# Kernel tuning notes

Measured on AMD Instinct MI355X. Metric: run time of the kernel, lower is better.

The kernel has to match this reference:

```python
import jax, jax.numpy as jnp
import numpy as np

PH, PW = 7, 7          # pooled_height, pooled_width
SCALE = 0.0625         # spatial_scale
K = 6                  # static max integer cells per bin side (max bin size = 448*SCALE/7 = 4)


def setup_inputs() -> dict:
    key = jax.random.key(0)
    kf, kb, kx, ky, kw, kh = jax.random.split(key, 6)
    B, C, H, W = 4, 256, 64, 64
    R = 1024
    features = jax.random.normal(kf, (B, C, H, W), dtype=jnp.float32)
    # rois rows: (batch_idx, x1, y1, x2, y2) in image coords (image ~1024px, scale 1/16)
    bidx = jax.random.randint(kb, (R,), 0, B).astype(jnp.float32)
    x1 = jax.random.uniform(kx, (R,), minval=0.0, maxval=576.0)
    y1 = jax.random.uniform(ky, (R,), minval=0.0, maxval=576.0)
    bw = jax.random.uniform(kw, (R,), minval=32.0, maxval=448.0)
    bh = jax.random.uniform(kh, (R,), minval=32.0, maxval=448.0)
    rois = jnp.stack([bidx, x1, y1, x1 + bw, y1 + bh], axis=1)
    return {"features": features, "rois": rois}


def _gather(features, b, hidx, widx, H, W):
    # hidx: [R,PH] int32, widx: [R,PW] int32 -> [R,PH,PW,C]; out-of-bounds reads are zero
    vh = (hidx >= 0) & (hidx < H)
    vw = (widx >= 0) & (widx < W)
    mask = (vh[:, :, None] & vw[:, None, :]).astype(features.dtype)  # [R,PH,PW]
    hc = jnp.clip(hidx, 0, H - 1)
    wc = jnp.clip(widx, 0, W - 1)
    d = features[b[:, None, None], :, hc[:, :, None], wc[:, None, :]]  # [R,PH,PW,C]
    return d * mask[..., None]


def _cell_weights(start, end, s):
    # exact integrals of the two 1D bilinear hat weights over [start,end] clipped to cell [s, s+1]
    y0 = jnp.maximum(start, s)
    yl = jnp.maximum(jnp.minimum(end, s + 1.0), y0)  # empty intersection -> zero weights
    a = y0 - s
    la = yl - s
    g0 = la - 0.5 * la * la - a + 0.5 * a * a  # weight of node at s
    g1 = 0.5 * la * la - 0.5 * a * a           # weight of node at s+1
    return g0, g1


def prroi_pool(features, rois):
    B, C, H, W = features.shape
    R = rois.shape[0]
    dt = features.dtype
    b = rois[:, 0].astype(jnp.int32)
    x1 = rois[:, 1] * SCALE
    y1 = rois[:, 2] * SCALE
    x2 = rois[:, 3] * SCALE
    y2 = rois[:, 4] * SCALE
    roi_w = jnp.maximum(x2 - x1, 0.0)
    roi_h = jnp.maximum(y2 - y1, 0.0)
    bin_w = roi_w / PW
    bin_h = roi_h / PH
    # per-bin continuous windows [ws, we)
    ws_w = x1[:, None] + bin_w[:, None] * jnp.arange(PW, dtype=dt)  # [R,PW]
    ws_h = y1[:, None] + bin_h[:, None] * jnp.arange(PH, dtype=dt)  # [R,PH]
    we_w = ws_w + bin_w[:, None]
    we_h = ws_h + bin_h[:, None]
    s0_w = jnp.floor(ws_w)
    s0_h = jnp.floor(ws_h)

    offs = np.stack(np.meshgrid(np.arange(K), np.arange(K), indexing="ij"), -1).reshape(-1, 2)
    offs = jnp.asarray(offs, dtype=dt)  # [K*K, 2] (dh, dw)

    def step(acc, off):
        sh = s0_h + off[0]  # [R,PH] float (integer-valued)
        sw = s0_w + off[1]  # [R,PW]
        gy0, gy1 = _cell_weights(ws_h, we_h, sh)
        gx0, gx1 = _cell_weights(ws_w, we_w, sw)
        hi = sh.astype(jnp.int32)
        wi = sw.astype(jnp.int32)
        d00 = _gather(features, b, hi, wi, H, W)
        d01 = _gather(features, b, hi, wi + 1, H, W)
        d10 = _gather(features, b, hi + 1, wi, H, W)
        d11 = _gather(features, b, hi + 1, wi + 1, H, W)
        gy0 = gy0[:, :, None, None]
        gy1 = gy1[:, :, None, None]
        gx0 = gx0[:, None, :, None]
        gx1 = gx1[:, None, :, None]
        contrib = d00 * (gy0 * gx0) + d01 * (gy0 * gx1) + d10 * (gy1 * gx0) + d11 * (gy1 * gx1)
        return acc + contrib, None

    acc0 = jnp.zeros((R, PH, PW, C), dtype=dt)
    acc, _ = jax.lax.scan(step, acc0, offs)
    win = (bin_w * bin_h)[:, None, None, None]  # bin area in feature coords
    out = jnp.where(win > 0, acc / jnp.where(win > 0, win, 1.0), 0.0)
    return jnp.transpose(out, (0, 3, 1, 2))  # [R, C, PH, PW]


def reference(features, rois):
    return prroi_pool(features, rois)
```

## Files before the change

kernel.cpp:

```cpp
#include <hip/hip_runtime.h>
#include <hip/hip_fp16.h>

#define R_    1024
#define B_    4
#define C_    256
#define H_    64
#define W_    64
#define HW_   4096
#define PHW_  49
#define ROIT  128
#define LROWF 258
#define SLACKH 17408

__device__ __forceinline__ void cell_w(float start, float end, float s, float& g0, float& g1) {
    float y0 = fmaxf(start, s);
    float yl = fmaxf(fminf(end, s + 1.0f), y0);
    float a  = y0 - s;
    float la = yl - s;
    g0 = la - 0.5f * la * la - a + 0.5f * a * a;
    g1 = 0.5f * la * la - 0.5f * a * a;
}

__device__ __forceinline__ void h8_fma(uint4 v, float w, float4& ga, float4& gb) {
    __half2 h0 = *(__half2*)&v.x, h1 = *(__half2*)&v.y;
    __half2 h2 = *(__half2*)&v.z, h3 = *(__half2*)&v.w;
    float2 f0 = __half22float2(h0), f1 = __half22float2(h1);
    float2 f2 = __half22float2(h2), f3 = __half22float2(h3);
    ga.x = fmaf(w, f0.x, ga.x); ga.y = fmaf(w, f0.y, ga.y);
    ga.z = fmaf(w, f1.x, ga.z); ga.w = fmaf(w, f1.y, ga.w);
    gb.x = fmaf(w, f2.x, gb.x); gb.y = fmaf(w, f2.y, gb.y);
    gb.z = fmaf(w, f3.x, gb.z); gb.w = fmaf(w, f3.y, gb.w);
}

__global__ __launch_bounds__(256) void prep(const float* __restrict__ in,
                                            __half* __restrict__ fTh,
                                            const float* __restrict__ rois,
                                            int* __restrict__ perm,
                                            float* __restrict__ roitab) {
    int bid = blockIdx.x;
    if (bid < 4096) {
        __shared__ float tile[32][33];
        int b   = bid >> 10;
        int rem = bid & 1023;
        int c0  = (rem >> 7) * 32;
        int p0  = (rem & 127) * 32;
        int tx  = threadIdx.x & 31;
        int ty  = threadIdx.x >> 5;
        const float* src = in + (size_t)b * C_ * HW_;
#pragma unroll
        for (int i = 0; i < 32; i += 8)
            tile[ty + i][tx] = src[(size_t)(c0 + ty + i) * HW_ + (p0 + tx)];
        __syncthreads();
        __half2* dsth = (__half2*)(fTh + (size_t)b * HW_ * C_);
#pragma unroll
        for (int i = 0; i < 2; ++i) {
            int idx = threadIdx.x + i * 256;
            int py  = idx >> 4;
            int cp  = idx & 15;
            float lo = tile[cp * 2][py];
            float hi = tile[cp * 2 + 1][py];
            dsth[(size_t)(p0 + py) * (C_ / 2) + (c0 >> 1) + cp] = __floats2half2_rn(lo, hi);
        }
        return;
    }
    if (bid == 4096) {
        if (threadIdx.x >= 64) {
            for (int j = threadIdx.x - 64; j < SLACKH; j += 192)
                fTh[(size_t)B_ * HW_ * C_ + j] = __half(0.0f);
            return;
        }
        int lane = threadIdx.x;
        unsigned long long below = (1ull << lane) - 1ull;
        int key[16];
#pragma unroll
        for (int i = 0; i < 16; ++i) {
            int idx = i * 64 + lane;
            const float* roi = rois + idx * 5;
            int b = (int)roi[0];
            float yc = (roi[2] + roi[4]) * 0.5f * 0.0625f;
            int yb = min(3, max(0, (int)(yc * 0.0625f)));
            key[i] = b * 4 + yb;
        }
        int cntk[16];
#pragma unroll
        for (int k = 0; k < 16; ++k) cntk[k] = 0;
        for (int i = 0; i < 16; ++i)
#pragma unroll
            for (int k = 0; k < 16; ++k)
                cntk[k] += __popcll(__ballot(key[i] == k));
        int off[16]; int acc = 0;
#pragma unroll
        for (int k = 0; k < 16; ++k) { off[k] = acc; acc += cntk[k]; }
        for (int i = 0; i < 16; ++i) {
#pragma unroll
            for (int k = 0; k < 16; ++k) {
                unsigned long long m = __ballot(key[i] == k);
                if (key[i] == k)
                    perm[off[k] + __popcll(m & below)] = i * 64 + lane;
                off[k] += __popcll(m);
            }
        }
        return;
    }
    int i = (bid - 4097) * 256 + threadIdx.x;
    int r  = i / PHW_;
    int k  = i - r * PHW_;
    int ph = k / 7, pw = k - ph * 7;
    const float* roi = rois + r * 5;
    int bb = (int)roi[0];
    float x1 = roi[1] * 0.0625f, y1 = roi[2] * 0.0625f;
    float x2 = roi[3] * 0.0625f, y2 = roi[4] * 0.0625f;
    float rw = fmaxf(x2 - x1, 0.0f), rh = fmaxf(y2 - y1, 0.0f);
    float bw = rw / 7.0f, bh = rh / 7.0f;
    float win = bw * bh;
    float* rt = roitab + (size_t)r * ROIT;

    float wy[8], wx[7];
#pragma unroll
    for (int t = 0; t < 7; ++t) { wy[t] = 0.0f; wx[t] = 0.0f; }
    wy[7] = 0.0f;
    int w0 = 0, h0 = 0, npy = 0, w00 = 0;
    float invwin = 0.0f;
    if (win > 0.0f) {
        float ws = x1 + bw * (float)pw, we = ws + bw;
        float hs = y1 + bh * (float)ph, he = hs + bh;
        float s0w = floorf(ws), s0h = floorf(hs);
        w0 = (int)s0w; h0 = (int)s0h;
        w00 = (int)floorf(x1);
#pragma unroll
        for (int o = 0; o < 6; ++o) {
            float g0, g1;
            cell_w(hs, he, s0h + (float)o, g0, g1);
            wy[o] += g0; wy[o + 1] += g1;
            cell_w(ws, we, s0w + (float)o, g0, g1);
            wx[o] += g0; wx[o + 1] += g1;
        }
        npy = min(7, max(0, (int)ceilf(he - s0h + 1.0f)));
        int npx = min(7, max(0, (int)ceilf(we - s0w + 1.0f)));
        npy = max(0, min(npy, H_ - h0));
        npx = max(0, min(npx, W_ - w0));
#pragma unroll
        for (int t = 0; t < 7; ++t) {
            if (t >= npx) wx[t] = 0.0f;
            if (t >= npy) wy[t] = 0.0f;
        }
        invwin = 1.0f / win;
    }
    if (ph == 0) {
#pragma unroll
        for (int t = 0; t < 7; ++t) rt[pw * 7 + t] = wx[t];
        rt[49 + pw] = __int_as_float(w0 - w00);
    }
    if (pw == 0) {
#pragma unroll
        for (int t = 0; t < 8; ++t) rt[72 + ph * 8 + t] = wy[t] * invwin;
        rt[64 + ph] = __int_as_float(h0 | (npy << 8));
    }
    if (k == 0) {
        int jlim = 0;
        if (win > 0.0f) {
#pragma unroll
            for (int p = 0; p < 7; ++p) {
                float wsp = x1 + bw * (float)p, wep = wsp + bw;
                float s0wp = floorf(wsp);
                int w0p = (int)s0wp;
                int npxp = min(7, max(0, (int)ceilf(wep - s0wp + 1.0f)));
                npxp = max(0, min(npxp, W_ - w0p));
                jlim = max(jlim, (w0p - w00) + npxp);
            }
        }
        rt[63] = __int_as_float(bb | (w00 << 8) | (jlim << 16));
    }
}

__global__ __launch_bounds__(256) void prroi_rows(const __half* __restrict__ fTh,
                                                  const int* __restrict__ perm,
                                                  const float* __restrict__ roitab,
                                                  __half* __restrict__ scr) {
    __shared__ __align__(16) float colw[4][32 * 8];
    int wid  = __builtin_amdgcn_readfirstlane(threadIdx.x >> 6);
    int lane = threadIdx.x & 63;
    float* cwv = colw[wid];
    int bid = blockIdx.x;
    int xcd = bid & 7;
    int s   = (bid >> 3) * 4 + wid;
    if (s >= 896) return;
    int t   = (s & 31) * 28 + (s >> 5);
    int g   = xcd * 896 + t;
    int rs  = g / 7;
    int ph  = g - rs * 7;
    int r   = __builtin_amdgcn_readfirstlane(perm[rs]);
    const float* rt = roitab + (size_t)r * ROIT;

#pragma unroll
    for (int u = 0; u < 4; ++u) cwv[lane + u * 64] = 0.0f;
    if (lane < 49) {
        int pw = lane / 7;
        int dx = lane - pw * 7;
        float wxv = rt[lane];
        int d = __float_as_int(rt[49 + pw]);
        cwv[(d + dx) * 8 + pw] = wxv;
    }
    int meta = __float_as_int(rt[63]);
    int bb   = meta & 0xff;
    int w00  = (meta >> 8) & 0xff;
    int jlim = (meta >> 16) & 0xff;
    int hm   = __float_as_int(rt[64 + ph]);
    int h0   = hm & 0xff;
    int npy  = (hm >> 8) & 0xff;
    int npy2 = (npy + 1) & ~1;
    const float* wyp = rt + 72 + ph * 8;

    int half = lane >> 5;
    int cl   = lane & 31;
    const __half* fr = fTh + ((size_t)bb * HW_ + (size_t)h0 * W_ + w00 + half) * C_ + cl * 8;

    float4 aA[7], aB[7];
#pragma unroll
    for (int p = 0; p < 7; ++p) {
        aA[p] = make_float4(0.f, 0.f, 0.f, 0.f);
        aB[p] = make_float4(0.f, 0.f, 0.f, 0.f);
    }

    for (int jl = 0; jl < jlim; jl += 2) {
        const float* cw = cwv + (jl + half) * 8;
        float4 c0 = *(const float4*)(cw);
        float4 c1 = *(const float4*)(cw + 4);
        const __half* cp = fr + (size_t)jl * C_;
        float4 gA = make_float4(0.f, 0.f, 0.f, 0.f);
        float4 gB = make_float4(0.f, 0.f, 0.f, 0.f);
        for (int dy = 0; dy < npy2; dy += 2) {
            const __half* r0 = cp + (size_t)dy * (W_ * C_);
            uint4 va = *(const uint4*)(r0);
            uint4 vb = *(const uint4*)(r0 + W_ * C_);
            float w0y = wyp[dy];
            float w1y = wyp[dy + 1];
            h8_fma(va, w0y, gA, gB);
            h8_fma(vb, w1y, gA, gB);
        }
#define APPLY(P, CP) { \
    aA[P].x = fmaf(CP, gA.x, aA[P].x); aA[P].y = fmaf(CP, gA.y, aA[P].y); \
    aA[P].z = fmaf(CP, gA.z, aA[P].z); aA[P].w = fmaf(CP, gA.w, aA[P].w); \
    aB[P].x = fmaf(CP, gB.x, aB[P].x); aB[P].y = fmaf(CP, gB.y, aB[P].y); \
    aB[P].z = fmaf(CP, gB.z, aB[P].z); aB[P].w = fmaf(CP, gB.w, aB[P].w); }
        APPLY(0, c0.x); APPLY(1, c0.y); APPLY(2, c0.z); APPLY(3, c0.w);
        APPLY(4, c1.x); APPLY(5, c1.y); APPLY(6, c1.z);
#undef APPLY
    }

#pragma unroll
    for (int p = 0; p < 7; ++p) {
        aA[p].x += __shfl_xor(aA[p].x, 32);
        aA[p].y += __shfl_xor(aA[p].y, 32);
        aA[p].z += __shfl_xor(aA[p].z, 32);
        aA[p].w += __shfl_xor(aA[p].w, 32);
        aB[p].x += __shfl_xor(aB[p].x, 32);
        aB[p].y += __shfl_xor(aB[p].y, 32);
        aB[p].z += __shfl_xor(aB[p].z, 32);
        aB[p].w += __shfl_xor(aB[p].w, 32);
    }

    __half* sb = scr + ((size_t)r * PHW_ + ph * 7) * C_ + cl * 8;
#pragma unroll
    for (int s4 = 0; s4 < 4; ++s4) {
        const int ihi = (4 + s4 > 6) ? 6 : 4 + s4;
        float4 pa = half ? aA[ihi] : aA[s4];
        float4 pb = half ? aB[ihi] : aB[s4];
        int p = half ? 4 + s4 : s4;
        if (p < 7) {
            union { __half2 h2[4]; uint4 u; } pk;
            pk.h2[0] = __floats2half2_rn(pa.x, pa.y);
            pk.h2[1] = __floats2half2_rn(pa.z, pa.w);
            pk.h2[2] = __floats2half2_rn(pb.x, pb.y);
            pk.h2[3] = __floats2half2_rn(pb.z, pb.w);
            *(uint4*)(sb + (size_t)p * C_) = pk.u;
        }
    }
}

__global__ __launch_bounds__(256) void fixup(const int* __restrict__ perm,
                                             const __half* __restrict__ scr,
                                             float* __restrict__ out) {
    __shared__ __align__(4) __half lds_h[PHW_ * LROWF];
    int bid  = blockIdx.x;
    int spos = ((bid & 7) << 7) | (bid >> 3);
    int r    = perm[spos];
    const unsigned int* src = (const unsigned int*)(scr + (size_t)r * PHW_ * C_);
    for (int j = threadIdx.x; j < PHW_ * (C_ / 2); j += 256) {
        int row = j >> 7;
        int col = j & 127;
        *(unsigned int*)&lds_h[row * LROWF + col * 2] = src[j];
    }
    __syncthreads();
    float* outr = out + (size_t)r * (C_ * PHW_);
#pragma unroll 4
    for (int j = threadIdx.x; j < C_ * PHW_; j += 256) {
        int c = j / PHW_;
        int k = j - c * PHW_;
        outr[j] = __half2float(lds_h[k * LROWF + c]);
    }
}

__global__ __launch_bounds__(256) void prroi_pool_direct(const float* __restrict__ f,
                                                         const float* __restrict__ rois,
                                                         float* __restrict__ out) {
    int bin = blockIdx.x;
    int r  = bin / PHW_;
    int k  = bin - r * PHW_;
    int ph = k / 7;
    int pw = k - ph * 7;
    int c = threadIdx.x;

    const float* roi = rois + r * 5;
    int bb = (int)roi[0];
    float x1 = roi[1] * 0.0625f, y1 = roi[2] * 0.0625f;
    float x2 = roi[3] * 0.0625f, y2 = roi[4] * 0.0625f;
    float rw = fmaxf(x2 - x1, 0.0f), rh = fmaxf(y2 - y1, 0.0f);
    float bw = rw / 7.0f, bh = rh / 7.0f;
    float win = bw * bh;
    size_t oidx = ((size_t)r * C_ + c) * PHW_ + k;
    if (!(win > 0.0f)) { out[oidx] = 0.0f; return; }

    float ws = x1 + bw * (float)pw, we = ws + bw;
    float hs = y1 + bh * (float)ph, he = hs + bh;
    float s0w = floorf(ws), s0h = floorf(hs);
    int w0 = (int)s0w, h0 = (int)s0h;
    float wy[7], wx[7];
#pragma unroll
    for (int t = 0; t < 7; ++t) { wy[t] = 0.0f; wx[t] = 0.0f; }
#pragma unroll
    for (int o = 0; o < 6; ++o) {
        float g0, g1;
        cell_w(hs, he, s0h + (float)o, g0, g1);
        wy[o] += g0; wy[o + 1] += g1;
        cell_w(ws, we, s0w + (float)o, g0, g1);
        wx[o] += g0; wx[o + 1] += g1;
    }
    int npy = min(7, max(0, (int)ceilf(he - s0h + 1.0f)));
    int npx = min(7, max(0, (int)ceilf(we - s0w + 1.0f)));
    npy = max(0, min(npy, H_ - h0));
    npx = max(0, min(npx, W_ - w0));

    const float* fbc = f + ((size_t)bb * C_ + c) * (H_ * W_);
    float acc = 0.0f;
#pragma unroll
    for (int dy = 0; dy < 7; ++dy) {
        if (dy < npy) {
            float row = 0.0f;
#pragma unroll
            for (int dx = 0; dx < 7; ++dx) {
                if (dx < npx)
                    row = fmaf(wx[dx], fbc[(h0 + dy) * W_ + (w0 + dx)], row);
            }
            acc = fmaf(wy[dy], row, acc);
        }
    }
    out[oidx] = acc / win;
}

extern "C" void kernel_launch(void* const* d_in, const int* in_sizes, int n_in,
                              void* d_out, int out_size, void* d_ws, size_t ws_size,
                              hipStream_t stream) {
    const float* feat = (const float*)d_in[0];
    const float* rois = (const float*)d_in[1];
    float* out = (float*)d_out;

    const size_t fth_b   = (size_t)B_ * HW_ * C_ * sizeof(__half);
    const size_t slack_b = (size_t)SLACKH * sizeof(__half);
    const size_t perm_b  = (size_t)R_ * sizeof(int);
    const size_t rt_b    = (size_t)R_ * ROIT * sizeof(float);
    const size_t scr_b   = (size_t)R_ * PHW_ * C_ * sizeof(__half);

    const size_t base = fth_b + slack_b + perm_b + rt_b;
    if (ws_size >= base + scr_b) {
        __half* fTh  = (__half*)d_ws;
        int*    perm = (int*)((char*)d_ws + fth_b + slack_b);
        float*  rtab = (float*)((char*)d_ws + fth_b + slack_b + perm_b);
        __half* scr  = (__half*)((char*)d_ws + base);
        prep<<<4293, 256, 0, stream>>>(feat, fTh, rois, perm, rtab);
        prroi_rows<<<2048, 256, 0, stream>>>(fTh, perm, rtab, scr);
        fixup<<<R_, 256, 0, stream>>>(perm, scr, out);
    } else {
        prroi_pool_direct<<<R_ * PHW_, 256, 0, stream>>>(feat, rois, out);
    }
}
```

Baseline: 63.38 us.

## Accumulate vertical sums with packed half FMA and split fixup per channel half

The inner vertical accumulation loop in prroi_rows now uses packed __hfma2 on half2 values and converts to float only once per column, rather than unpacking every loaded value to float and doing scalar FMAs. Separately, the fixup transpose kernel is split into two blocks per ROI, each handling 128 channels with a smaller LDS tile, which doubles the block count and cuts shared memory per block. The half-precision accumulation adds rounding error to the intermediate sums, and the fixup change raises occupancy but adds more block launches.

```diff
diff --git a/kernel.cpp b/kernel.cpp
--- a/kernel.cpp
+++ b/kernel.cpp
@@ -9,7 +9,7 @@
 #define HW_   4096
 #define PHW_  49
 #define ROIT  128
-#define LROWF 258
+#define LROWH 130
 #define SLACKH 17408
 
 __device__ __forceinline__ void cell_w(float start, float end, float s, float& g0, float& g1) {
@@ -19,17 +19,6 @@
     float la = yl - s;
     g0 = la - 0.5f * la * la - a + 0.5f * a * a;
     g1 = 0.5f * la * la - 0.5f * a * a;
-}
-
-__device__ __forceinline__ void h8_fma(uint4 v, float w, float4& ga, float4& gb) {
-    __half2 h0 = *(__half2*)&v.x, h1 = *(__half2*)&v.y;
-    __half2 h2 = *(__half2*)&v.z, h3 = *(__half2*)&v.w;
-    float2 f0 = __half22float2(h0), f1 = __half22float2(h1);
-    float2 f2 = __half22float2(h2), f3 = __half22float2(h3);
-    ga.x = fmaf(w, f0.x, ga.x); ga.y = fmaf(w, f0.y, ga.y);
-    ga.z = fmaf(w, f1.x, ga.z); ga.w = fmaf(w, f1.y, ga.w);
-    gb.x = fmaf(w, f2.x, gb.x); gb.y = fmaf(w, f2.y, gb.y);
-    gb.z = fmaf(w, f3.x, gb.z); gb.w = fmaf(w, f3.y, gb.w);
 }
 
 __global__ __launch_bounds__(256) void prep(const float* __restrict__ in,
@@ -227,17 +216,28 @@
         float4 c0 = *(const float4*)(cw);
         float4 c1 = *(const float4*)(cw + 4);
         const __half* cp = fr + (size_t)jl * C_;
-        float4 gA = make_float4(0.f, 0.f, 0.f, 0.f);
-        float4 gB = make_float4(0.f, 0.f, 0.f, 0.f);
+        __half2 g0 = __float2half2_rn(0.0f), g1 = g0, g2 = g0, g3 = g0;
         for (int dy = 0; dy < npy2; dy += 2) {
             const __half* r0 = cp + (size_t)dy * (W_ * C_);
             uint4 va = *(const uint4*)(r0);
             uint4 vb = *(const uint4*)(r0 + W_ * C_);
-            float w0y = wyp[dy];
-            float w1y = wyp[dy + 1];
-            h8_fma(va, w0y, gA, gB);
-            h8_fma(vb, w1y, gA, gB);
-        }
+            __half2 w0h = __float2half2_rn(wyp[dy]);
+            __half2 w1h = __float2half2_rn(wyp[dy + 1]);
+            g0 = __hfma2(w0h, *(__half2*)&va.x, g0);
+            g1 = __hfma2(w0h, *(__half2*)&va.y, g1);
+            g2 = __hfma2(w0h, *(__half2*)&va.z, g2);
+            g3 = __hfma2(w0h, *(__half2*)&va.w, g3);
+            g0 = __hfma2(w1h, *(__half2*)&vb.x, g0);
+            g1 = __hfma2(w1h, *(__half2*)&vb.y, g1);
+            g2 = __hfma2(w1h, *(__half2*)&vb.z, g2);
+            g3 = __hfma2(w1h, *(__half2*)&vb.w, g3);
+        }
+        float2 t0 = __half22float2(g0);
+        float2 t1 = __half22float2(g1);
+        float2 t2 = __half22float2(g2);
+        float2 t3 = __half22float2(g3);
+        float4 gA = make_float4(t0.x, t0.y, t1.x, t1.y);
+        float4 gB = make_float4(t2.x, t2.y, t3.x, t3.y);
 #define APPLY(P, CP) { \
     aA[P].x = fmaf(CP, gA.x, aA[P].x); aA[P].y = fmaf(CP, gA.y, aA[P].y); \
     aA[P].z = fmaf(CP, gA.z, aA[P].z); aA[P].w = fmaf(CP, gA.w, aA[P].w); \
@@ -281,23 +281,25 @@
 __global__ __launch_bounds__(256) void fixup(const int* __restrict__ perm,
                                              const __half* __restrict__ scr,
                                              float* __restrict__ out) {
-    __shared__ __align__(4) __half lds_h[PHW_ * LROWF];
+    __shared__ __align__(4) __half lds_h[PHW_ * LROWH];
     int bid  = blockIdx.x;
-    int spos = ((bid & 7) << 7) | (bid >> 3);
-    int r    = perm[spos];
-    const unsigned int* src = (const unsigned int*)(scr + (size_t)r * PHW_ * C_);
-    for (int j = threadIdx.x; j < PHW_ * (C_ / 2); j += 256) {
-        int row = j >> 7;
-        int col = j & 127;
-        *(unsigned int*)&lds_h[row * LROWF + col * 2] = src[j];
+    int idx  = (bid & 7) * 256 + (bid >> 3);
+    int rs   = idx >> 1;
+    int half = idx & 1;
+    int r    = perm[rs];
+    const unsigned int* src = (const unsigned int*)(scr + (size_t)r * PHW_ * C_ + half * 128);
+    for (int j = threadIdx.x; j < PHW_ * 64; j += 256) {
+        int row = j >> 6;
+        int col = j & 63;
+        *(unsigned int*)&lds_h[row * LROWH + col * 2] = src[(size_t)row * (C_ / 2) + col];
     }
     __syncthreads();
-    float* outr = out + (size_t)r * (C_ * PHW_);
+    float* outr = out + (size_t)r * (C_ * PHW_) + (size_t)half * 128 * PHW_;
 #pragma unroll 4
-    for (int j = threadIdx.x; j < C_ * PHW_; j += 256) {
+    for (int j = threadIdx.x; j < 128 * PHW_; j += 256) {
         int c = j / PHW_;
         int k = j - c * PHW_;
-        outr[j] = __half2float(lds_h[k * LROWF + c]);
+        outr[j] = __half2float(lds_h[k * LROWH + c]);
     }
 }
 
@@ -379,7 +381,7 @@
         __half* scr  = (__half*)((char*)d_ws + base);
         prep<<<4293, 256, 0, stream>>>(feat, fTh, rois, perm, rtab);
         prroi_rows<<<2048, 256, 0, stream>>>(fTh, perm, rtab, scr);
-        fixup<<<R_, 256, 0, stream>>>(perm, scr, out);
+        fixup<<<2048, 256, 0, stream>>>(perm, scr, out);
     } else {
         prroi_pool_direct<<<R_ * PHW_, 256, 0, stream>>>(feat, rois, out);
     }
```

New measurement: 61.21 us. 1.04x faster.
